# Optimization experiments

Hardware: AMD Instinct MI355X
Metric: run time of the kernel (lower is better)

Reference implementation:

```python
import jax, jax.numpy as jnp
import numpy as np

B, S, D, F, E = 4, 2048, 1024, 4096, 8
LN_EPS = 1e-5


def setup_inputs() -> dict:
    key = jax.random.key(0)
    ks = jax.random.split(key, 6)
    sc = 0.02
    return {
        "x": jax.random.normal(ks[0], (B, S, D), dtype=jnp.float32),
        "Wr": jax.random.normal(ks[1], (D, E), dtype=jnp.float32) * sc,
        "br": jnp.zeros((E,), jnp.float32),
        "ln_g": jnp.ones((D,), jnp.float32),
        "ln_b": jnp.zeros((D,), jnp.float32),
        "W1": jax.random.normal(ks[2], (E, D, F), dtype=jnp.float32) * sc,
        "b1": jnp.zeros((E, F), jnp.float32),
        "W2": jax.random.normal(ks[3], (E, F, D), dtype=jnp.float32) * sc,
        "b2": jnp.zeros((E, D), jnp.float32),
    }


def reference(x, Wr, br, ln_g, ln_b, W1, b1, W2, b2):
    tokens_shape = x.shape[:-1]
    xt = x.reshape(-1, x.shape[-1])  # [T, D]

    # top-1 routing (eval mode: no jitter noise, no dropout)
    router_logits = xt @ Wr + br                      # [T, E]
    router_probs = jax.nn.softmax(router_logits, axis=-1)
    gates = jnp.max(router_probs, axis=-1, keepdims=True)   # [T, 1]
    idx = jnp.argmax(router_probs, axis=-1)                 # [T] int
    onehot = jax.nn.one_hot(idx, E, dtype=xt.dtype)         # [T, E]

    # layernorm
    mu = jnp.mean(xt, axis=-1, keepdims=True)
    var = jnp.mean(jnp.square(xt - mu), axis=-1, keepdims=True)
    xn = (xt - mu) * jax.lax.rsqrt(var + LN_EPS) * ln_g + ln_b

    # expert FFN: per-token expert-specific GEMMs expressed via one-hot dispatch
    h = jnp.einsum('te,td,edf->tf', onehot, xn, W1) + b1[idx]  # [T, F]
    h = jax.nn.relu(h)
    y = jnp.einsum('te,tf,efd->td', onehot, h, W2) + b2[idx]   # [T, D]

    y = y * gates
    return y.reshape(tokens_shape + (y.shape[-1],))
```

## Files before the change

### kernel.cpp

```cpp
#include <hip/hip_runtime.h>
#include <stdint.h>

#define T_TOK 8192
#define DDIM  1024
#define FDIM  4096
#define NEXP  8
#define BM 128
#define BK 64
#define MAX_MT (T_TOK / BM + NEXP)

typedef __attribute__((ext_vector_type(8))) short bf16x8;
typedef __attribute__((ext_vector_type(8))) unsigned short u16x8;
typedef __attribute__((ext_vector_type(4))) float f32x4;

__device__ __forceinline__ unsigned short f2bf(float f) {
    union { float f; unsigned u; } v; v.f = f;
    unsigned u = v.u;
    u += 0x7fffu + ((u >> 16) & 1u);
    return (unsigned short)(u >> 16);
}

__device__ __forceinline__ void async16(const void* g, void* l) {
    __builtin_amdgcn_global_load_lds(
        (const __attribute__((address_space(1))) unsigned int*)g,
        (__attribute__((address_space(3))) unsigned int*)l, 16, 0, 0);
}

__global__ __launch_bounds__(256) void init_kernel(
    const float* __restrict__ Wr, float* __restrict__ WrT, int* __restrict__ meta) {
    int idx = blockIdx.x * 256 + threadIdx.x;
    if (idx < 16) meta[idx] = 0;
    float v = Wr[idx];
    WrT[(idx & 7) * DDIM + (idx >> 3)] = v;
}

__global__ __launch_bounds__(256) void prep(
    const float* __restrict__ x, const float* __restrict__ WrT, const float* __restrict__ br,
    const float* __restrict__ lng, const float* __restrict__ lnb,
    const float* __restrict__ W1, const float* __restrict__ W2,
    unsigned short* __restrict__ xn, unsigned short* __restrict__ W1t,
    unsigned short* __restrict__ W2t, float* __restrict__ gate,
    int* __restrict__ expert, int* __restrict__ counts, float* __restrict__ y) {
    __shared__ float smem[64 * 65];
    int b = blockIdx.x, tid = threadIdx.x;
    int r4 = b & 3, q = b >> 2;

    if (r4 == 3) {
        float4 z = make_float4(0.f, 0.f, 0.f, 0.f);
        ((float4*)y)[(size_t)q * 256 + tid] = z;
        return;
    }
    if (r4 != 0) {
        const float* src; unsigned short* dst; int R, C, e, c0, r0;
        if (r4 == 1) {
            R = DDIM; C = FDIM;
            e = q >> 10;
            c0 = (q & 63) * 64; r0 = ((q >> 6) & 15) * 64;
            src = W1; dst = W1t;
        } else {
            R = FDIM; C = DDIM;
            e = q >> 10;
            c0 = (q & 15) * 64; r0 = ((q >> 4) & 63) * 64;
            src = W2; dst = W2t;
        }
        const float* s = src + (size_t)e * R * C;
        unsigned short* d = dst + (size_t)e * R * C;
        float (*tile)[65] = (float(*)[65])smem;
        int lr = tid >> 4, lc = (tid & 15) * 4;
#pragma unroll
        for (int i = 0; i < 4; i++) {
            float4 v = *(const float4*)&s[(size_t)(r0 + lr + i * 16) * C + c0 + lc];
            tile[lr + i * 16][lc + 0] = v.x;
            tile[lr + i * 16][lc + 1] = v.y;
            tile[lr + i * 16][lc + 2] = v.z;
            tile[lr + i * 16][lc + 3] = v.w;
        }
        __syncthreads();
#pragma unroll
        for (int i = 0; i < 2; i++) {
            int ix = tid + i * 256;
            int drow = ix >> 3, seg = ix & 7;
            u16x8 o;
#pragma unroll
            for (int j = 0; j < 8; j++) o[j] = f2bf(tile[seg * 8 + j][drow]);
            *(u16x8*)&d[(size_t)(c0 + drow) * R + r0 + seg * 8] = o;
        }
        return;
    }

    int t = q;
    const float* xrow = x + (size_t)t * DDIM;
    float4 xv = ((const float4*)xrow)[tid];
    float s  = xv.x + xv.y + xv.z + xv.w;
    float sq = xv.x * xv.x + xv.y * xv.y + xv.z * xv.z + xv.w * xv.w;
    ((float2*)smem)[tid] = make_float2(s, sq);

    int e = tid >> 5, l32 = tid & 31;
    const float* wrow = WrT + e * DDIM + l32;
    const float* xp = xrow + l32;
    float a0 = 0, a1 = 0, a2 = 0, a3 = 0;
#pragma unroll
    for (int j = 0; j < 32; j += 4) {
        a0 += xp[32 * j]       * wrow[32 * j];
        a1 += xp[32 * (j + 1)] * wrow[32 * (j + 1)];
        a2 += xp[32 * (j + 2)] * wrow[32 * (j + 2)];
        a3 += xp[32 * (j + 3)] * wrow[32 * (j + 3)];
    }
    float acc = (a0 + a1) + (a2 + a3);
#pragma unroll
    for (int o = 16; o > 0; o >>= 1) acc += __shfl_down(acc, o, 32);
    if ((tid & 31) == 0) smem[512 + e] = acc;
    __syncthreads();

    if (tid < 64) {
        float2 p0 = ((float2*)smem)[tid];
        float2 p1 = ((float2*)smem)[tid + 64];
        float2 p2 = ((float2*)smem)[tid + 128];
        float2 p3 = ((float2*)smem)[tid + 192];
        float ss = (p0.x + p1.x) + (p2.x + p3.x);
        float qq = (p0.y + p1.y) + (p2.y + p3.y);
#pragma unroll
        for (int o = 32; o > 0; o >>= 1) {
            ss += __shfl_down(ss, o);
            qq += __shfl_down(qq, o);
        }
        if (tid == 0) {
            float mu = ss * (1.f / DDIM);
            float var = qq * (1.f / DDIM) - mu * mu;
            float rstd = rsqrtf(var + 1e-5f);
            int best = 0; float bl = -3.4e38f;
            float L[8];
            for (int k = 0; k < 8; k++) {
                float l = smem[512 + k] + br[k];
                L[k] = l;
                if (l > bl) { bl = l; best = k; }
            }
            float den = 0;
            for (int k = 0; k < 8; k++) den += __expf(L[k] - bl);
            gate[t] = 1.f / den;
            expert[t] = best;
            atomicAdd(&counts[best], 1);
            smem[520] = mu; smem[521] = rstd;
        }
    }
    __syncthreads();
    float mu = smem[520], rstd = smem[521];
    float4 gg = ((const float4*)lng)[tid];
    float4 bb = ((const float4*)lnb)[tid];
    ushort4 o;
    o.x = f2bf((xv.x - mu) * rstd * gg.x + bb.x);
    o.y = f2bf((xv.y - mu) * rstd * gg.y + bb.y);
    o.z = f2bf((xv.z - mu) * rstd * gg.z + bb.z);
    o.w = f2bf((xv.w - mu) * rstd * gg.w + bb.w);
    *(ushort4*)(xn + (size_t)t * DDIM + tid * 4) = o;
}

__global__ __launch_bounds__(256) void scatter_perm(
    const int* __restrict__ expert, const int* __restrict__ counts,
    int* __restrict__ fill, int* __restrict__ perm) {
    __shared__ int offs_s[NEXP];
    if (threadIdx.x < NEXP) {
        int o = 0;
        for (int i = 0; i < (int)threadIdx.x; i++) o += counts[i];
        offs_s[threadIdx.x] = o;
    }
    __syncthreads();
    int t = blockIdx.x * 256 + threadIdx.x;
    int e = expert[t];
    int p = atomicAdd(&fill[e], 1);
    perm[offs_s[e] + p] = t;
}

template <int MODE>
__global__ __launch_bounds__(256) void gemm_grouped(
    const unsigned short* __restrict__ A, const unsigned short* __restrict__ Bt,
    const float* __restrict__ bias, unsigned short* __restrict__ Hout,
    float* __restrict__ Yout, const float* __restrict__ gate,
    const int* __restrict__ perm, const int* __restrict__ counts,
    int K, int N) {
    int rem = blockIdx.x;
    int e, off = 0, cnt = 0; bool found = false;
    for (e = 0; e < NEXP; e++) {
        cnt = counts[e];
        int mt = (cnt + (BM - 1)) >> 7;
        if (rem < mt) { found = true; break; }
        rem -= mt; off += cnt;
    }
    if (!found) return;
    int mbase = rem << 7;
    int mrem = cnt - mbase;
    int n0, kbase, kend, kh;
    if (MODE == 0) {
        n0 = blockIdx.y << 7; kbase = 0; kend = K; kh = 0;
    } else {
        n0 = (blockIdx.y >> 1) << 7;
        kh = blockIdx.y & 1;
        kbase = kh * (K >> 1); kend = kbase + (K >> 1);
    }

    __shared__ __align__(16) unsigned short Alds[BM * BK];
    __shared__ __align__(16) unsigned short Blds[128 * BK];

    int tid = threadIdx.x;
    int lane = tid & 63, wave = tid >> 6;
    int grow = lane >> 3;
    int seg  = lane & 7;
    int gseg = seg ^ grow;

    const unsigned short* ag[4];
    unsigned short* al[4];
    const unsigned short* bg[4];
    unsigned short* bl[4];
#pragma unroll
    for (int p = 0; p < 4; p++) {
        int r = p * 32 + wave * 8 + grow;
        int rr = (r < mrem) ? r : 0;
        int t = (MODE == 0) ? perm[off + mbase + rr] : (off + mbase + rr);
        ag[p] = A + (size_t)t * K + gseg * 8;
        al[p] = &Alds[(p * 32 + wave * 8) * BK];
        bg[p] = Bt + ((size_t)e * N + n0 + r) * K + gseg * 8;
        bl[p] = &Blds[(p * 32 + wave * 8) * BK];
    }

    int wr = (wave >> 1) * 64, wc = (wave & 1) * 64;
    int q = lane >> 4, l16 = lane & 15;
    int sx = l16 & 7;

    f32x4 acc[4][4] = {};

    for (int k0 = kbase; k0 < kend; k0 += BK) {
#pragma unroll
        for (int p = 0; p < 4; p++) async16(ag[p] + k0, al[p]);
#pragma unroll
        for (int p = 0; p < 4; p++) async16(bg[p] + k0, bl[p]);
        __syncthreads();
#pragma unroll
        for (int kk = 0; kk < 2; kk++) {
            int slot = ((kk * 4 + q) ^ sx) * 8;
            bf16x8 af[4], bfr[4];
#pragma unroll
            for (int i = 0; i < 4; i++)
                af[i] = *(const bf16x8*)&Alds[(wr + i * 16 + l16) * BK + slot];
#pragma unroll
            for (int j = 0; j < 4; j++)
                bfr[j] = *(const bf16x8*)&Blds[(wc + j * 16 + l16) * BK + slot];
#pragma unroll
            for (int i = 0; i < 4; i++)
#pragma unroll
                for (int j = 0; j < 4; j++)
                    acc[i][j] = __builtin_amdgcn_mfma_f32_16x16x32_bf16(af[i], bfr[j], acc[i][j], 0, 0, 0);
        }
        __syncthreads();
    }

    float bs[4];
#pragma unroll
    for (int j = 0; j < 4; j++) bs[j] = bias[(size_t)e * N + n0 + wc + j * 16 + l16];
#pragma unroll
    for (int i = 0; i < 4; i++) {
#pragma unroll
        for (int r = 0; r < 4; r++) {
            int lrow = wr + i * 16 + q * 4 + r;
            if (lrow < mrem) {
                if (MODE == 0) {
                    unsigned short* hp = Hout + (size_t)(off + mbase + lrow) * N + n0 + wc + l16;
#pragma unroll
                    for (int j = 0; j < 4; j++) {
                        float v = acc[i][j][r] + bs[j];
                        hp[j * 16] = f2bf(fmaxf(v, 0.f));
                    }
                } else {
                    int t = perm[off + mbase + lrow];
                    float gt = gate[t];
                    float* yp = Yout + (size_t)t * N + n0 + wc + l16;
#pragma unroll
                    for (int j = 0; j < 4; j++) {
                        float v = (acc[i][j][r] + (kh ? 0.f : bs[j])) * gt;
                        atomicAdd(&yp[j * 16], v);
                    }
                }
            }
        }
    }
}

extern "C" void kernel_launch(void* const* d_in, const int* in_sizes, int n_in,
                              void* d_out, int out_size, void* d_ws, size_t ws_size,
                              hipStream_t stream) {
    const float* x   = (const float*)d_in[0];
    const float* Wr  = (const float*)d_in[1];
    const float* br  = (const float*)d_in[2];
    const float* lng = (const float*)d_in[3];
    const float* lnb = (const float*)d_in[4];
    const float* W1  = (const float*)d_in[5];
    const float* b1  = (const float*)d_in[6];
    const float* W2  = (const float*)d_in[7];
    const float* b2  = (const float*)d_in[8];
    float* out = (float*)d_out;

    char* ws = (char*)d_ws;
    size_t o = 0;
    unsigned short* W1t = (unsigned short*)(ws + o); o += (size_t)NEXP * DDIM * FDIM * 2;
    unsigned short* W2t = (unsigned short*)(ws + o); o += (size_t)NEXP * DDIM * FDIM * 2;
    unsigned short* xn  = (unsigned short*)(ws + o); o += (size_t)T_TOK * DDIM * 2;
    unsigned short* h   = (unsigned short*)(ws + o); o += (size_t)T_TOK * FDIM * 2;
    float* gate = (float*)(ws + o); o += (size_t)T_TOK * 4;
    float* WrT  = (float*)(ws + o); o += (size_t)NEXP * DDIM * 4;
    int* expert = (int*)(ws + o);   o += (size_t)T_TOK * 4;
    int* perm   = (int*)(ws + o);   o += (size_t)T_TOK * 4;
    int* meta   = (int*)(ws + o);
    int* counts = meta;
    int* fill   = meta + 8;

    init_kernel<<<32, 256, 0, stream>>>(Wr, WrT, meta);
    prep<<<4 * T_TOK, 256, 0, stream>>>(x, WrT, br, lng, lnb, W1, W2,
                                        xn, W1t, W2t, gate, expert, counts, out);
    scatter_perm<<<T_TOK / 256, 256, 0, stream>>>(expert, counts, fill, perm);
    gemm_grouped<0><<<dim3(MAX_MT, FDIM / 128), 256, 0, stream>>>(
        xn, W1t, b1, h, nullptr, nullptr, perm, counts, DDIM, FDIM);
    gemm_grouped<1><<<dim3(MAX_MT, (DDIM / 128) * 2), 256, 0, stream>>>(
        h, W2t, b2, nullptr, out, gate, perm, counts, FDIM, DDIM);
}
```

Before: 666.9 us.

## Overlap W2 transpose with first GEMM and drop split-K atomics in second GEMM

Moves the W2 fp32-to-bf16 transpose out of the prep kernel and into extra blocks of the first grouped GEMM launch, so that conversion work can run alongside GEMM tiles. The output zero-fill and the split-K atomicAdd epilogue of the second GEMM are removed. In their place, each block now covers the full K with a 64-wide N tile and writes the output directly. This trades atomic traffic and the memset for less per-block parallelism along K and a longer K loop per block in the second GEMM.

```diff
diff --git a/kernel.cpp b/kernel.cpp
--- a/kernel.cpp
+++ b/kernel.cpp
@@ -8,6 +8,8 @@
 #define BM 128
 #define BK 64
 #define MAX_MT (T_TOK / BM + NEXP)
+#define G0_TILES (MAX_MT * (FDIM / 128))
+#define W2_TILES 8192
 
 typedef __attribute__((ext_vector_type(8))) short bf16x8;
 typedef __attribute__((ext_vector_type(8))) unsigned short u16x8;
@@ -24,6 +26,33 @@
     __builtin_amdgcn_global_load_lds(
         (const __attribute__((address_space(1))) unsigned int*)g,
         (__attribute__((address_space(3))) unsigned int*)l, 16, 0, 0);
+}
+
+__device__ __forceinline__ void transpose_tile64(
+    float* smem, const float* __restrict__ src, unsigned short* __restrict__ dst,
+    int R, int C, int e, int r0, int c0, int tid) {
+    const float* s = src + (size_t)e * R * C;
+    unsigned short* d = dst + (size_t)e * R * C;
+    float (*tile)[65] = (float(*)[65])smem;
+    int lr = tid >> 4, lc = (tid & 15) * 4;
+#pragma unroll
+    for (int i = 0; i < 4; i++) {
+        float4 v = *(const float4*)&s[(size_t)(r0 + lr + i * 16) * C + c0 + lc];
+        tile[lr + i * 16][lc + 0] = v.x;
+        tile[lr + i * 16][lc + 1] = v.y;
+        tile[lr + i * 16][lc + 2] = v.z;
+        tile[lr + i * 16][lc + 3] = v.w;
+    }
+    __syncthreads();
+#pragma unroll
+    for (int i = 0; i < 2; i++) {
+        int ix = tid + i * 256;
+        int drow = ix >> 3, seg = ix & 7;
+        u16x8 o;
+#pragma unroll
+        for (int j = 0; j < 8; j++) o[j] = f2bf(tile[seg * 8 + j][drow]);
+        *(u16x8*)&d[(size_t)(c0 + drow) * R + r0 + seg * 8] = o;
+    }
 }
 
 __global__ __launch_bounds__(256) void init_kernel(
@@ -37,54 +66,17 @@
 __global__ __launch_bounds__(256) void prep(
     const float* __restrict__ x, const float* __restrict__ WrT, const float* __restrict__ br,
     const float* __restrict__ lng, const float* __restrict__ lnb,
-    const float* __restrict__ W1, const float* __restrict__ W2,
+    const float* __restrict__ W1,
     unsigned short* __restrict__ xn, unsigned short* __restrict__ W1t,
-    unsigned short* __restrict__ W2t, float* __restrict__ gate,
-    int* __restrict__ expert, int* __restrict__ counts, float* __restrict__ y) {
+    float* __restrict__ gate, int* __restrict__ expert, int* __restrict__ counts) {
     __shared__ float smem[64 * 65];
     int b = blockIdx.x, tid = threadIdx.x;
-    int r4 = b & 3, q = b >> 2;
-
-    if (r4 == 3) {
-        float4 z = make_float4(0.f, 0.f, 0.f, 0.f);
-        ((float4*)y)[(size_t)q * 256 + tid] = z;
-        return;
-    }
-    if (r4 != 0) {
-        const float* src; unsigned short* dst; int R, C, e, c0, r0;
-        if (r4 == 1) {
-            R = DDIM; C = FDIM;
-            e = q >> 10;
-            c0 = (q & 63) * 64; r0 = ((q >> 6) & 15) * 64;
-            src = W1; dst = W1t;
-        } else {
-            R = FDIM; C = DDIM;
-            e = q >> 10;
-            c0 = (q & 15) * 64; r0 = ((q >> 4) & 63) * 64;
-            src = W2; dst = W2t;
-        }
-        const float* s = src + (size_t)e * R * C;
-        unsigned short* d = dst + (size_t)e * R * C;
-        float (*tile)[65] = (float(*)[65])smem;
-        int lr = tid >> 4, lc = (tid & 15) * 4;
-#pragma unroll
-        for (int i = 0; i < 4; i++) {
-            float4 v = *(const float4*)&s[(size_t)(r0 + lr + i * 16) * C + c0 + lc];
-            tile[lr + i * 16][lc + 0] = v.x;
-            tile[lr + i * 16][lc + 1] = v.y;
-            tile[lr + i * 16][lc + 2] = v.z;
-            tile[lr + i * 16][lc + 3] = v.w;
-        }
-        __syncthreads();
-#pragma unroll
-        for (int i = 0; i < 2; i++) {
-            int ix = tid + i * 256;
-            int drow = ix >> 3, seg = ix & 7;
-            u16x8 o;
-#pragma unroll
-            for (int j = 0; j < 8; j++) o[j] = f2bf(tile[seg * 8 + j][drow]);
-            *(u16x8*)&d[(size_t)(c0 + drow) * R + r0 + seg * 8] = o;
-        }
+    int r2 = b & 1, q = b >> 1;
+
+    if (r2 == 1) {
+        int e = q >> 10;
+        int c0 = (q & 63) * 64, r0 = ((q >> 6) & 15) * 64;
+        transpose_tile64(smem, W1, W1t, DDIM, FDIM, e, r0, c0, tid);
         return;
     }
 
@@ -171,13 +163,117 @@
     perm[offs_s[e] + p] = t;
 }
 
-template <int MODE>
-__global__ __launch_bounds__(256) void gemm_grouped(
+__global__ __launch_bounds__(256) void gemm0_w2t(
     const unsigned short* __restrict__ A, const unsigned short* __restrict__ Bt,
     const float* __restrict__ bias, unsigned short* __restrict__ Hout,
-    float* __restrict__ Yout, const float* __restrict__ gate,
-    const int* __restrict__ perm, const int* __restrict__ counts,
-    int K, int N) {
+    const float* __restrict__ W2, unsigned short* __restrict__ W2t,
+    const int* __restrict__ perm, const int* __restrict__ counts) {
+    __shared__ __align__(16) unsigned short smem_u[16384];
+    int tid = threadIdx.x;
+
+    if (blockIdx.x >= G0_TILES) {
+        int q = blockIdx.x - G0_TILES;
+        int e = q >> 10;
+        int c0 = (q & 15) * 64, r0 = ((q >> 4) & 63) * 64;
+        transpose_tile64((float*)smem_u, W2, W2t, FDIM, DDIM, e, r0, c0, tid);
+        return;
+    }
+
+    const int K = DDIM, N = FDIM;
+    int bx = blockIdx.x;
+    int rem = bx >> 5;
+    int n0 = (bx & 31) << 7;
+    int e, off = 0, cnt = 0; bool found = false;
+    for (e = 0; e < NEXP; e++) {
+        cnt = counts[e];
+        int mt = (cnt + (BM - 1)) >> 7;
+        if (rem < mt) { found = true; break; }
+        rem -= mt; off += cnt;
+    }
+    if (!found) return;
+    int mbase = rem << 7;
+    int mrem = cnt - mbase;
+
+    unsigned short* Alds = smem_u;
+    unsigned short* Blds = smem_u + 8192;
+
+    int lane = tid & 63, wave = tid >> 6;
+    int grow = lane >> 3;
+    int seg  = lane & 7;
+    int gseg = seg ^ grow;
+
+    const unsigned short* ag[4];
+    unsigned short* al[4];
+    const unsigned short* bg[4];
+    unsigned short* bl[4];
+#pragma unroll
+    for (int p = 0; p < 4; p++) {
+        int r = p * 32 + wave * 8 + grow;
+        int rr = (r < mrem) ? r : 0;
+        int t = perm[off + mbase + rr];
+        ag[p] = A + (size_t)t * K + gseg * 8;
+        al[p] = &Alds[(p * 32 + wave * 8) * BK];
+        bg[p] = Bt + ((size_t)e * N + n0 + r) * K + gseg * 8;
+        bl[p] = &Blds[(p * 32 + wave * 8) * BK];
+    }
+
+    int wr = (wave >> 1) * 64, wc = (wave & 1) * 64;
+    int q = lane >> 4, l16 = lane & 15;
+    int sx = l16 & 7;
+
+    f32x4 acc[4][4] = {};
+
+    for (int k0 = 0; k0 < K; k0 += BK) {
+#pragma unroll
+        for (int p = 0; p < 4; p++) async16(ag[p] + k0, al[p]);
+#pragma unroll
+        for (int p = 0; p < 4; p++) async16(bg[p] + k0, bl[p]);
+        __syncthreads();
+#pragma unroll
+        for (int kk = 0; kk < 2; kk++) {
+            int slot = ((kk * 4 + q) ^ sx) * 8;
+            bf16x8 af[4], bfr[4];
+#pragma unroll
+            for (int i = 0; i < 4; i++)
+                af[i] = *(const bf16x8*)&Alds[(wr + i * 16 + l16) * BK + slot];
+#pragma unroll
+            for (int j = 0; j < 4; j++)
+                bfr[j] = *(const bf16x8*)&Blds[(wc + j * 16 + l16) * BK + slot];
+#pragma unroll
+            for (int i = 0; i < 4; i++)
+#pragma unroll
+                for (int j = 0; j < 4; j++)
+                    acc[i][j] = __builtin_amdgcn_mfma_f32_16x16x32_bf16(af[i], bfr[j], acc[i][j], 0, 0, 0);
+        }
+        __syncthreads();
+    }
+
+    float bs[4];
+#pragma unroll
+    for (int j = 0; j < 4; j++) bs[j] = bias[(size_t)e * N + n0 + wc + j * 16 + l16];
+#pragma unroll
+    for (int i = 0; i < 4; i++) {
+#pragma unroll
+        for (int r = 0; r < 4; r++) {
+            int lrow = wr + i * 16 + q * 4 + r;
+            if (lrow < mrem) {
+                unsigned short* hp = Hout + (size_t)(off + mbase + lrow) * N + n0 + wc + l16;
+#pragma unroll
+                for (int j = 0; j < 4; j++) {
+                    float v = acc[i][j][r] + bs[j];
+                    hp[j * 16] = f2bf(fmaxf(v, 0.f));
+                }
+            }
+        }
+    }
+}
+
+__global__ __launch_bounds__(256) void gemm1(
+    const unsigned short* __restrict__ A, const unsigned short* __restrict__ Bt,
+    const float* __restrict__ bias, float* __restrict__ Yout,
+    const float* __restrict__ gate, const int* __restrict__ perm,
+    const int* __restrict__ counts) {
+    const int K = FDIM, N = DDIM;
     int rem = blockIdx.x;
     int e, off = 0, cnt = 0; bool found = false;
     for (e = 0; e < NEXP; e++) {
@@ -189,17 +285,10 @@
     if (!found) return;
     int mbase = rem << 7;
     int mrem = cnt - mbase;
-    int n0, kbase, kend, kh;
-    if (MODE == 0) {
-        n0 = blockIdx.y << 7; kbase = 0; kend = K; kh = 0;
-    } else {
-        n0 = (blockIdx.y >> 1) << 7;
-        kh = blockIdx.y & 1;
-        kbase = kh * (K >> 1); kend = kbase + (K >> 1);
-    }
+    int n0 = blockIdx.y << 6;
 
     __shared__ __align__(16) unsigned short Alds[BM * BK];
-    __shared__ __align__(16) unsigned short Blds[128 * BK];
+    __shared__ __align__(16) unsigned short Blds[64 * BK];
 
     int tid = threadIdx.x;
     int lane = tid & 63, wave = tid >> 6;
@@ -209,43 +298,46 @@
 
     const unsigned short* ag[4];
     unsigned short* al[4];
-    const unsigned short* bg[4];
-    unsigned short* bl[4];
+    const unsigned short* bg[2];
+    unsigned short* bl[2];
 #pragma unroll
     for (int p = 0; p < 4; p++) {
         int r = p * 32 + wave * 8 + grow;
         int rr = (r < mrem) ? r : 0;
-        int t = (MODE == 0) ? perm[off + mbase + rr] : (off + mbase + rr);
-        ag[p] = A + (size_t)t * K + gseg * 8;
+        ag[p] = A + (size_t)(off + mbase + rr) * K + gseg * 8;
         al[p] = &Alds[(p * 32 + wave * 8) * BK];
+    }
+#pragma unroll
+    for (int p = 0; p < 2; p++) {
+        int r = p * 32 + wave * 8 + grow;
         bg[p] = Bt + ((size_t)e * N + n0 + r) * K + gseg * 8;
         bl[p] = &Blds[(p * 32 + wave * 8) * BK];
     }
 
-    int wr = (wave >> 1) * 64, wc = (wave & 1) * 64;
+    int wr = wave * 32, wc = 0;
     int q = lane >> 4, l16 = lane & 15;
     int sx = l16 & 7;
 
-    f32x4 acc[4][4] = {};
-
-    for (int k0 = kbase; k0 < kend; k0 += BK) {
+    f32x4 acc[2][4] = {};
+
+    for (int k0 = 0; k0 < K; k0 += BK) {
 #pragma unroll
         for (int p = 0; p < 4; p++) async16(ag[p] + k0, al[p]);
 #pragma unroll
-        for (int p = 0; p < 4; p++) async16(bg[p] + k0, bl[p]);
+        for (int p = 0; p < 2; p++) async16(bg[p] + k0, bl[p]);
         __syncthreads();
 #pragma unroll
         for (int kk = 0; kk < 2; kk++) {
             int slot = ((kk * 4 + q) ^ sx) * 8;
-            bf16x8 af[4], bfr[4];
-#pragma unroll
-            for (int i = 0; i < 4; i++)
+            bf16x8 af[2], bfr[4];
+#pragma unroll
+            for (int i = 0; i < 2; i++)
                 af[i] = *(const bf16x8*)&Alds[(wr + i * 16 + l16) * BK + slot];
 #pragma unroll
             for (int j = 0; j < 4; j++)
                 bfr[j] = *(const bf16x8*)&Blds[(wc + j * 16 + l16) * BK + slot];
 #pragma unroll
-            for (int i = 0; i < 4; i++)
+            for (int i = 0; i < 2; i++)
 #pragma unroll
                 for (int j = 0; j < 4; j++)
                     acc[i][j] = __builtin_amdgcn_mfma_f32_16x16x32_bf16(af[i], bfr[j], acc[i][j], 0, 0, 0);
@@ -257,28 +349,17 @@
 #pragma unroll
     for (int j = 0; j < 4; j++) bs[j] = bias[(size_t)e * N + n0 + wc + j * 16 + l16];
 #pragma unroll
-    for (int i = 0; i < 4; i++) {
+    for (int i = 0; i < 2; i++) {
 #pragma unroll
         for (int r = 0; r < 4; r++) {
             int lrow = wr + i * 16 + q * 4 + r;
             if (lrow < mrem) {
-                if (MODE == 0) {
-                    unsigned short* hp = Hout + (size_t)(off + mbase + lrow) * N + n0 + wc + l16;
-#pragma unroll
-                    for (int j = 0; j < 4; j++) {
-                        float v = acc[i][j][r] + bs[j];
-                        hp[j * 16] = f2bf(fmaxf(v, 0.f));
-                    }
-                } else {
-                    int t = perm[off + mbase + lrow];
-                    float gt = gate[t];
-                    float* yp = Yout + (size_t)t * N + n0 + wc + l16;
-#pragma unroll
-                    for (int j = 0; j < 4; j++) {
-                        float v = (acc[i][j][r] + (kh ? 0.f : bs[j])) * gt;
-                        atomicAdd(&yp[j * 16], v);
-                    }
-                }
+                int t = perm[off + mbase + lrow];
+                float gt = gate[t];
+                float* yp = Yout + (size_t)t * N + n0 + wc + l16;
+#pragma unroll
+                for (int j = 0; j < 4; j++)
+                    yp[j * 16] = (acc[i][j][r] + bs[j]) * gt;
             }
         }
     }
@@ -313,11 +394,11 @@
     int* fill   = meta + 8;
 
     init_kernel<<<32, 256, 0, stream>>>(Wr, WrT, meta);
-    prep<<<4 * T_TOK, 256, 0, stream>>>(x, WrT, br, lng, lnb, W1, W2,
-                                        xn, W1t, W2t, gate, expert, counts, out);
+    prep<<<2 * T_TOK, 256, 0, stream>>>(x, WrT, br, lng, lnb, W1,
+                                        xn, W1t, gate, expert, counts);
     scatter_perm<<<T_TOK / 256, 256, 0, stream>>>(expert, counts, fill, perm);
-    gemm_grouped<0><<<dim3(MAX_MT, FDIM / 128), 256, 0, stream>>>(
-        xn, W1t, b1, h, nullptr, nullptr, perm, counts, DDIM, FDIM);
-    gemm_grouped<1><<<dim3(MAX_MT, (DDIM / 128) * 2), 256, 0, stream>>>(
-        h, W2t, b2, nullptr, out, gate, perm, counts, FDIM, DDIM);
-}
+    gemm0_w2t<<<G0_TILES + W2_TILES, 256, 0, stream>>>(
+        xn, W1t, b1, h, W2, W2t, perm, counts);
+    gemm1<<<dim3(MAX_MT, DDIM / 64), 256, 0, stream>>>(
+        h, W2t, b2, out, gate, perm, counts);
+}
```

New measurement: 620.1 us. 7.0% less time.
